# Kernel tuning notes

Measured on AMD Instinct MI355X. Metric: run time of the kernel, lower is better.

## Reference

```python
import jax, jax.numpy as jnp
import numpy as np

B, N, H = 2, 2048, 1024
NUM_HEADS = 16
HEAD_DIM = H // NUM_HEADS
SCALE = HEAD_DIM ** -0.5


def setup_inputs() -> dict:
    key = jax.random.key(0)
    k1, k2, k3, k4 = jax.random.split(key, 4)
    s = 0.02
    return {
        "x": jax.random.normal(k1, (B, N, H), dtype=jnp.float32),
        "x2": jax.random.normal(k2, (B, N, H), dtype=jnp.float32),
        "Wqkv": jax.random.normal(k3, (H, 3 * H), dtype=jnp.float32) * s,
        "Wout": jax.random.normal(k4, (H, H), dtype=jnp.float32) * s,
        "bout": jnp.zeros((H,), dtype=jnp.float32),
    }


def _split_qkv(t):
    # t: [B, N, 3H] -> [3, B, h, N, d]
    b, n, _ = t.shape
    t = t.reshape(b, n, 3, NUM_HEADS, HEAD_DIM)
    return jnp.transpose(t, (2, 0, 3, 1, 4))


def reference(x, x2, Wqkv, Wout, bout):
    # shared qkv projection applied to both streams (bias=False)
    qkv2 = _split_qkv(x2 @ Wqkv)  # k, v from x2
    k, v = qkv2[1], qkv2[2]       # [B, h, N2, d]
    qkv1 = _split_qkv(x @ Wqkv)   # q from x
    q = qkv1[0]                   # [B, h, N, d]

    att = jax.nn.softmax(jnp.einsum("bhxd,bhyd->bhxy", q, k) * SCALE, axis=-1)
    out = jnp.einsum("bhxy,bhyd->bhxd", att, v)        # [B, h, N, d]
    out = jnp.transpose(out, (0, 2, 1, 3)).reshape(x.shape[0], x.shape[1], -1)
    return out @ Wout + bout
```

## Files before the change

kernel.cpp:

```cpp
#include <hip/hip_runtime.h>

#define B_ 2
#define N_ 2048
#define H_ 1024
#define NH_ 16
#define D_ 64

typedef _Float16 f16;
typedef _Float16 f16x4 __attribute__((ext_vector_type(4)));
typedef _Float16 f16x8 __attribute__((ext_vector_type(8)));
typedef float f32x4 __attribute__((ext_vector_type(4)));

#define MFMA16(a, b, c) __builtin_amdgcn_mfma_f32_16x16x32_f16((a), (b), (c), 0, 0, 0)
#define MFMA16K(a, b, c) __builtin_amdgcn_mfma_f32_16x16x16f16((a), (b), (c), 0, 0, 0)

__device__ __forceinline__ void cp16(void* lds, const void* g) {
  __builtin_amdgcn_global_load_lds(
      (const __attribute__((address_space(1))) void*)g,
      (__attribute__((address_space(3))) void*)lds, 16, 0, 0);
}

__global__ __launch_bounds__(256) void convf16(
    const float* __restrict__ a, const float* __restrict__ b,
    f16* __restrict__ ao, f16* __restrict__ bo) {
  const size_t i = ((size_t)blockIdx.x * 256 + threadIdx.x) * 8;
  const float* __restrict__ src = (blockIdx.y == 0) ? a : b;
  f16* __restrict__ dst = (blockIdx.y == 0) ? ao : bo;
  float4 v0 = ((const float4*)(src + i))[0];
  float4 v1 = ((const float4*)(src + i))[1];
  f16x8 o;
  o[0] = (f16)v0.x; o[1] = (f16)v0.y; o[2] = (f16)v0.z; o[3] = (f16)v0.w;
  o[4] = (f16)v1.x; o[5] = (f16)v1.y; o[6] = (f16)v1.z; o[7] = (f16)v1.w;
  *(f16x8*)(dst + i) = o;
}

__global__ __launch_bounds__(256) void transw(
    const float* __restrict__ W, f16* __restrict__ Wt, int rows, int ncols) {
  const int cb = blockIdx.x * 64, kb = blockIdx.y * 64;
  const int t = threadIdx.x;
  __shared__ f16 T[64][72];
  {
    const int k = t >> 2, c0 = (t & 3) * 16;
    const float* wp = W + (size_t)(kb + k) * ncols + cb + c0;
    float4 w0 = ((const float4*)wp)[0];
    float4 w1 = ((const float4*)wp)[1];
    float4 w2 = ((const float4*)wp)[2];
    float4 w3 = ((const float4*)wp)[3];
    T[c0 + 0][k] = (f16)w0.x;  T[c0 + 1][k] = (f16)w0.y;
    T[c0 + 2][k] = (f16)w0.z;  T[c0 + 3][k] = (f16)w0.w;
    T[c0 + 4][k] = (f16)w1.x;  T[c0 + 5][k] = (f16)w1.y;
    T[c0 + 6][k] = (f16)w1.z;  T[c0 + 7][k] = (f16)w1.w;
    T[c0 + 8][k] = (f16)w2.x;  T[c0 + 9][k] = (f16)w2.y;
    T[c0 + 10][k] = (f16)w2.z; T[c0 + 11][k] = (f16)w2.w;
    T[c0 + 12][k] = (f16)w3.x; T[c0 + 13][k] = (f16)w3.y;
    T[c0 + 14][k] = (f16)w3.z; T[c0 + 15][k] = (f16)w3.w;
  }
  __syncthreads();
  {
    const int c = t >> 2, k0 = (t & 3) * 16;
    f16* op = Wt + (size_t)(cb + c) * rows + kb + k0;
    *(f16x8*)(op + 0) = *(const f16x8*)(&T[c][k0]);
    *(f16x8*)(op + 8) = *(const f16x8*)(&T[c][k0 + 8]);
  }
}

__global__ __launch_bounds__(256) void transv(
    const f16* __restrict__ V, f16* __restrict__ Vt) {
  const int nb = blockIdx.x * 64, bh = blockIdx.y;
  const int t = threadIdx.x;
  __shared__ f16 T[64][72];
  {
    const int n = t >> 2, d0 = (t & 3) * 16;
    const f16* vp = V + ((size_t)bh * N_ + nb + n) * D_ + d0;
    f16x8 v0 = *(const f16x8*)(vp);
    f16x8 v1 = *(const f16x8*)(vp + 8);
#pragma unroll
    for (int i = 0; i < 8; ++i) T[d0 + i][n] = v0[i];
#pragma unroll
    for (int i = 0; i < 8; ++i) T[d0 + 8 + i][n] = v1[i];
  }
  __syncthreads();
  {
    const int d = t >> 2, n0 = (t & 3) * 16;
    f16* op = Vt + ((size_t)bh * D_ + d) * N_ + nb + n0;
    *(f16x8*)(op + 0) = *(const f16x8*)(&T[d][n0]);
    *(f16x8*)(op + 8) = *(const f16x8*)(&T[d][n0 + 8]);
  }
}

__global__ __launch_bounds__(256) void qkv_mfma(
    const f16* __restrict__ Xc, const f16* __restrict__ X2c,
    const f16* __restrict__ Wt, f16* __restrict__ Qo,
    f16* __restrict__ Ko, f16* __restrict__ Vo) {
  const int bid = blockIdx.x;
  const int rb = (bid & 31) * 128;
  const int cb = (bid >> 5) * 128;
  const int t = threadIdx.x;
  const int lane = t & 63, wid = t >> 6;
  const int quad = lane >> 4, n16 = lane & 15;
  const int wm = wid >> 1, wn = wid & 1;

  const f16* __restrict__ A = (cb < H_) ? Xc : X2c;
  const int seg = cb >> 10;
  const float qscale = (seg == 0) ? 0.125f * 1.44269504f : 1.0f;
  f16* __restrict__ outp = (seg == 0) ? Qo : (seg == 1 ? Ko : Vo);

  __shared__ f16 As[128 * 32];
  __shared__ f16 Bs[128 * 32];

  f32x4 acc[4][4];
#pragma unroll
  for (int i = 0; i < 4; ++i)
#pragma unroll
    for (int j = 0; j < 4; ++j) acc[i][j] = (f32x4){0.f, 0.f, 0.f, 0.f};

  int srow0 = wid * 16 + (lane >> 2);
  int srow1 = 64 + srow0;
  int gl0 = ((lane & 3) ^ ((srow0 >> 1) & 3)) * 8;
  int gl1 = ((lane & 3) ^ ((srow1 >> 1) & 3)) * 8;
  const f16* gA0 = A + (size_t)(rb + srow0) * H_ + gl0;
  const f16* gA1 = A + (size_t)(rb + srow1) * H_ + gl1;
  const f16* gB0 = Wt + (size_t)(cb + srow0) * H_ + gl0;
  const f16* gB1 = Wt + (size_t)(cb + srow1) * H_ + gl1;
  f16* lA0 = &As[wid * 512];
  f16* lA1 = &As[2048 + wid * 512];
  f16* lB0 = &Bs[wid * 512];
  f16* lB1 = &Bs[2048 + wid * 512];

  const int fsw = (quad ^ ((n16 >> 1) & 3)) * 8;
  int aoff[4], boff[4];
#pragma unroll
  for (int i = 0; i < 4; ++i) {
    aoff[i] = (wm * 64 + i * 16 + n16) * 32 + fsw;
    boff[i] = (wn * 64 + i * 16 + n16) * 32 + fsw;
  }

  for (int kt = 0; kt < H_; kt += 32) {
    __syncthreads();
    cp16(lA0, gA0); cp16(lA1, gA1);
    cp16(lB0, gB0); cp16(lB1, gB1);
    gA0 += 32; gA1 += 32; gB0 += 32; gB1 += 32;
    __syncthreads();

    f16x8 af[4], bf[4];
#pragma unroll
    for (int mt = 0; mt < 4; ++mt) af[mt] = *(const f16x8*)(&As[aoff[mt]]);
#pragma unroll
    for (int nt = 0; nt < 4; ++nt) bf[nt] = *(const f16x8*)(&Bs[boff[nt]]);
#pragma unroll
    for (int mt = 0; mt < 4; ++mt)
#pragma unroll
      for (int nt = 0; nt < 4; ++nt)
        acc[mt][nt] = MFMA16(af[mt], bf[nt], acc[mt][nt]);
  }

#pragma unroll
  for (int mt = 0; mt < 4; ++mt)
#pragma unroll
    for (int nt = 0; nt < 4; ++nt)
#pragma unroll
      for (int r = 0; r < 4; ++r) {
        int grow = rb + wm * 64 + mt * 16 + quad * 4 + r;
        int gcol = cb + wn * 64 + nt * 16 + n16;
        int bb = grow >> 11, nn = grow & 2047;
        int hh = (gcol >> 6) & 15, dd = gcol & 63;
        outp[(((size_t)(bb * NH_ + hh)) * N_ + nn) * D_ + dd] =
            (f16)(acc[mt][nt][r] * qscale);
      }
}

__global__ __launch_bounds__(256) void attn4(
    const f16* __restrict__ Q, const f16* __restrict__ K,
    const f16* __restrict__ Vt, f16* __restrict__ AO) {
  const int bh = blockIdx.y;
  const int b = bh >> 4, h = bh & 15;
  const int qb = blockIdx.x * 64;
  const int t = threadIdx.x;
  const int lane = t & 63, wid = t >> 6;
  const int quad = lane >> 4, n16 = lane & 15;
  const int qh = wid & 1;
  const int kh = wid >> 1;

  const f16* __restrict__ Qp = Q + (size_t)bh * N_ * D_;
  const f16* __restrict__ Kp = K + (size_t)bh * N_ * D_;
  const f16* __restrict__ Vp = Vt + (size_t)bh * D_ * N_;

  __shared__ f16 Ks[2][64 * 64];
  __shared__ f16 Vs[2][64 * 64];

  f16x8 qf[2][2];
#pragma unroll
  for (int qc = 0; qc < 2; ++qc) {
    const f16* qp = Qp + (size_t)(qb + qh * 32 + qc * 16 + n16) * D_ + quad * 8;
    qf[qc][0] = *(const f16x8*)(qp);
    qf[qc][1] = *(const f16x8*)(qp + 32);
  }

  f32x4 o[2][4];
#pragma unroll
  for (int i = 0; i < 2; ++i)
#pragma unroll
    for (int j = 0; j < 4; ++j) o[i][j] = (f32x4){0.f, 0.f, 0.f, 0.f};
  float lsum[2] = {0.f, 0.f};

  const int srow0 = wid * 8 + (lane >> 3);
  const int srow1 = 32 + srow0;
  const int gl0 = ((lane & 7) ^ (srow0 & 7)) * 8;
  const int gl1 = ((lane & 7) ^ (srow1 & 7)) * 8;
  const f16* gK0 = Kp + (size_t)srow0 * D_ + gl0;
  const f16* gK1 = Kp + (size_t)srow1 * D_ + gl1;
  const f16* gV0 = Vp + (size_t)srow0 * N_ + gl0;
  const f16* gV1 = Vp + (size_t)srow1 * N_ + gl1;

  const int fs0 = (quad ^ (n16 & 7)) * 8;
  const int fs1 = ((quad + 4) ^ (n16 & 7)) * 8;
  int voff[4];
#pragma unroll
  for (int kc = 0; kc < 4; ++kc)
    voff[kc] = n16 * 64 + (((kc * 2 + (quad >> 1)) ^ (n16 & 7)) * 8) + (quad & 1) * 4;

  const f16* __restrict__ ks = &Ks[kh][0];
  const f16* __restrict__ vs = &Vs[kh][0];

  for (int kt = 0; kt < N_; kt += 128) {
    __syncthreads();
    cp16(&Ks[0][wid * 512], gK0 + (size_t)kt * D_);
    cp16(&Ks[0][2048 + wid * 512], gK1 + (size_t)kt * D_);
    cp16(&Ks[1][wid * 512], gK0 + (size_t)(kt + 64) * D_);
    cp16(&Ks[1][2048 + wid * 512], gK1 + (size_t)(kt + 64) * D_);
    cp16(&Vs[0][wid * 512], gV0 + kt);
    cp16(&Vs[0][2048 + wid * 512], gV1 + kt);
    cp16(&Vs[1][wid * 512], gV0 + kt + 64);
    cp16(&Vs[1][2048 + wid * 512], gV1 + kt + 64);
    __syncthreads();

    f32x4 s[2][4];
#pragma unroll
    for (int kc = 0; kc < 4; ++kc) {
      const f16x8 kf0 = *(const f16x8*)(&ks[(kc * 16 + n16) * 64 + fs0]);
      const f16x8 kf1 = *(const f16x8*)(&ks[(kc * 16 + n16) * 64 + fs1]);
#pragma unroll
      for (int qc = 0; qc < 2; ++qc) {
        f32x4 sv = (f32x4){0.f, 0.f, 0.f, 0.f};
        sv = MFMA16(kf0, qf[qc][0], sv);
        sv = MFMA16(kf1, qf[qc][1], sv);
        s[qc][kc] = sv;
      }
    }

    f16x4 pa[2][4];
#pragma unroll
    for (int qc = 0; qc < 2; ++qc)
#pragma unroll
      for (int kc = 0; kc < 4; ++kc)
#pragma unroll
        for (int r = 0; r < 4; ++r) {
          float p = __builtin_amdgcn_exp2f(s[qc][kc][r]);
          lsum[qc] += p;
          pa[qc][kc][r] = (f16)p;
        }

#pragma unroll
    for (int kc = 0; kc < 4; ++kc)
#pragma unroll
      for (int dt = 0; dt < 4; ++dt) {
        const f16x4 vb = *(const f16x4*)(&vs[dt * 1024 + voff[kc]]);
        o[0][dt] = MFMA16K(pa[0][kc], vb, o[0][dt]);
        o[1][dt] = MFMA16K(pa[1][kc], vb, o[1][dt]);
      }
  }

  __syncthreads();
  float* red = (float*)&Ks[0][0];
  if (kh == 1) {
    float* p = red + ((size_t)qh * 64 + lane) * 36;
#pragma unroll
    for (int qc = 0; qc < 2; ++qc)
#pragma unroll
      for (int dt = 0; dt < 4; ++dt)
        *(f32x4*)(p + (qc * 4 + dt) * 4) = o[qc][dt];
    p[32] = lsum[0];
    p[33] = lsum[1];
  }
  __syncthreads();
  if (kh == 0) {
    const float* p = red + ((size_t)qh * 64 + lane) * 36;
#pragma unroll
    for (int qc = 0; qc < 2; ++qc)
#pragma unroll
      for (int dt = 0; dt < 4; ++dt) {
        f32x4 v = *(const f32x4*)(p + (qc * 4 + dt) * 4);
#pragma unroll
        for (int r = 0; r < 4; ++r) o[qc][dt][r] += v[r];
      }
    lsum[0] += p[32];
    lsum[1] += p[33];

#pragma unroll
    for (int qc = 0; qc < 2; ++qc) {
      lsum[qc] += __shfl_xor(lsum[qc], 16);
      lsum[qc] += __shfl_xor(lsum[qc], 32);
    }

#pragma unroll
    for (int qc = 0; qc < 2; ++qc)
#pragma unroll
      for (int r = 0; r < 4; ++r) {
        float inv = 1.0f / __shfl(lsum[qc], quad * 4 + r);
        int nrow = qb + qh * 32 + qc * 16 + quad * 4 + r;
        f16* aop = AO + ((size_t)(b * N_ + nrow)) * H_ + h * 64;
#pragma unroll
        for (int dt = 0; dt < 4; ++dt)
          aop[dt * 16 + n16] = (f16)(o[qc][dt][r] * inv);
      }
  }
}

__global__ __launch_bounds__(256) void out_mfma(
    const f16* __restrict__ A, const f16* __restrict__ Wt,
    const float* __restrict__ bias, float* __restrict__ out) {
  const int bid = blockIdx.x;
  const int rb = (bid & 31) * 128;
  const int cb = (bid >> 5) * 128;
  const int t = threadIdx.x;
  const int lane = t & 63, wid = t >> 6;
  const int quad = lane >> 4, n16 = lane & 15;
  const int wm = wid >> 1, wn = wid & 1;

  __shared__ f16 As[128 * 32];
  __shared__ f16 Bs[128 * 32];

  f32x4 acc[4][4];
#pragma unroll
  for (int i = 0; i < 4; ++i)
#pragma unroll
    for (int j = 0; j < 4; ++j) acc[i][j] = (f32x4){0.f, 0.f, 0.f, 0.f};

  int srow0 = wid * 16 + (lane >> 2);
  int srow1 = 64 + srow0;
  int gl0 = ((lane & 3) ^ ((srow0 >> 1) & 3)) * 8;
  int gl1 = ((lane & 3) ^ ((srow1 >> 1) & 3)) * 8;
  const f16* gA0 = A + (size_t)(rb + srow0) * H_ + gl0;
  const f16* gA1 = A + (size_t)(rb + srow1) * H_ + gl1;
  const f16* gB0 = Wt + (size_t)(cb + srow0) * H_ + gl0;
  const f16* gB1 = Wt + (size_t)(cb + srow1) * H_ + gl1;
  f16* lA0 = &As[wid * 512];
  f16* lA1 = &As[2048 + wid * 512];
  f16* lB0 = &Bs[wid * 512];
  f16* lB1 = &Bs[2048 + wid * 512];

  const int fsw = (quad ^ ((n16 >> 1) & 3)) * 8;
  int aoff[4], boff[4];
#pragma unroll
  for (int i = 0; i < 4; ++i) {
    aoff[i] = (wm * 64 + i * 16 + n16) * 32 + fsw;
    boff[i] = (wn * 64 + i * 16 + n16) * 32 + fsw;
  }

  for (int kt = 0; kt < H_; kt += 32) {
    __syncthreads();
    cp16(lA0, gA0); cp16(lA1, gA1);
    cp16(lB0, gB0); cp16(lB1, gB1);
    gA0 += 32; gA1 += 32; gB0 += 32; gB1 += 32;
    __syncthreads();

    f16x8 af[4], bf[4];
#pragma unroll
    for (int mt = 0; mt < 4; ++mt) af[mt] = *(const f16x8*)(&As[aoff[mt]]);
#pragma unroll
    for (int nt = 0; nt < 4; ++nt) bf[nt] = *(const f16x8*)(&Bs[boff[nt]]);
#pragma unroll
    for (int mt = 0; mt < 4; ++mt)
#pragma unroll
      for (int nt = 0; nt < 4; ++nt)
        acc[mt][nt] = MFMA16(af[mt], bf[nt], acc[mt][nt]);
  }

#pragma unroll
  for (int nt = 0; nt < 4; ++nt) {
    int gcol = cb + wn * 64 + nt * 16 + n16;
    float bv = bias[gcol];
#pragma unroll
    for (int mt = 0; mt < 4; ++mt)
#pragma unroll
      for (int r = 0; r < 4; ++r) {
        int grow = rb + wm * 64 + mt * 16 + quad * 4 + r;
        out[(size_t)grow * H_ + gcol] = acc[mt][nt][r] + bv;
      }
  }
}

extern "C" void kernel_launch(void* const* d_in, const int* in_sizes, int n_in,
                              void* d_out, int out_size, void* d_ws, size_t ws_size,
                              hipStream_t stream) {
  const float* x    = (const float*)d_in[0];
  const float* x2   = (const float*)d_in[1];
  const float* Wqkv = (const float*)d_in[2];
  const float* Wout = (const float*)d_in[3];
  const float* bout = (const float*)d_in[4];
  float* out = (float*)d_out;

  const size_t per = (size_t)B_ * NH_ * N_ * D_;
  f16* Xc    = (f16*)d_ws;
  f16* X2c   = Xc + per;
  f16* Qw    = X2c + per;
  f16* Kw    = Qw + per;
  f16* Vw    = Kw + per;
  f16* Vtw   = Vw + per;
  f16* AO    = Vtw + per;
  f16* WqkvT = AO + per;
  f16* WoutT = WqkvT + (size_t)3072 * 1024;

  convf16<<<dim3(2048, 2), 256, 0, stream>>>(x, x2, Xc, X2c);
  transw<<<dim3(48, 16), 256, 0, stream>>>(Wqkv, WqkvT, H_, 3 * H_);
  transw<<<dim3(16, 16), 256, 0, stream>>>(Wout, WoutT, H_, H_);
  qkv_mfma<<<dim3(768), 256, 0, stream>>>(Xc, X2c, WqkvT, Qw, Kw, Vw);
  transv<<<dim3(32, 32), 256, 0, stream>>>(Vw, Vtw);
  attn4<<<dim3(32, 32), 256, 0, stream>>>(Qw, Kw, Vtw, AO);
  out_mfma<<<dim3(256), 256, 0, stream>>>(AO, WoutT, bout, out);
}
```

Baseline: 217.9 us.

## Merge prep kernels, emit transposed V from QKV GEMM, MFMA row sums in attention

```diff
diff --git a/kernel.cpp b/kernel.cpp
--- a/kernel.cpp
+++ b/kernel.cpp
@@ -7,6 +7,7 @@
 #define D_ 64
 
 typedef _Float16 f16;
+typedef _Float16 f16x2 __attribute__((ext_vector_type(2)));
 typedef _Float16 f16x4 __attribute__((ext_vector_type(4)));
 typedef _Float16 f16x8 __attribute__((ext_vector_type(8)));
 typedef float f32x4 __attribute__((ext_vector_type(4)));
@@ -20,24 +21,48 @@
       (__attribute__((address_space(3))) void*)lds, 16, 0, 0);
 }
 
-__global__ __launch_bounds__(256) void convf16(
-    const float* __restrict__ a, const float* __restrict__ b,
-    f16* __restrict__ ao, f16* __restrict__ bo) {
-  const size_t i = ((size_t)blockIdx.x * 256 + threadIdx.x) * 8;
-  const float* __restrict__ src = (blockIdx.y == 0) ? a : b;
-  f16* __restrict__ dst = (blockIdx.y == 0) ? ao : bo;
-  float4 v0 = ((const float4*)(src + i))[0];
-  float4 v1 = ((const float4*)(src + i))[1];
-  f16x8 o;
-  o[0] = (f16)v0.x; o[1] = (f16)v0.y; o[2] = (f16)v0.z; o[3] = (f16)v0.w;
-  o[4] = (f16)v1.x; o[5] = (f16)v1.y; o[6] = (f16)v1.z; o[7] = (f16)v1.w;
-  *(f16x8*)(dst + i) = o;
-}
-
-__global__ __launch_bounds__(256) void transw(
-    const float* __restrict__ W, f16* __restrict__ Wt, int rows, int ncols) {
-  const int cb = blockIdx.x * 64, kb = blockIdx.y * 64;
+__device__ __forceinline__ f16x4 pk4(float a, float b, float c, float d) {
+  auto lo = __builtin_amdgcn_cvt_pkrtz(a, b);
+  auto hi = __builtin_amdgcn_cvt_pkrtz(c, d);
+  f16x4 r;
+  r[0] = (f16)lo[0]; r[1] = (f16)lo[1]; r[2] = (f16)hi[0]; r[3] = (f16)hi[1];
+  return r;
+}
+
+__global__ __launch_bounds__(256) void prep(
+    const float* __restrict__ x, const float* __restrict__ x2,
+    f16* __restrict__ xo, f16* __restrict__ x2o,
+    const float* __restrict__ Wqkv, f16* __restrict__ WqkvT,
+    const float* __restrict__ Wout, f16* __restrict__ WoutT) {
+  const int bid = blockIdx.x;
   const int t = threadIdx.x;
+
+  if (bid < 4096) {
+    const float* __restrict__ src = (bid < 2048) ? x : x2;
+    f16* __restrict__ dst = (bid < 2048) ? xo : x2o;
+    const size_t i = ((size_t)(bid & 2047) * 256 + t) * 8;
+    float4 v0 = ((const float4*)(src + i))[0];
+    float4 v1 = ((const float4*)(src + i))[1];
+    f16x8 o;
+    o[0] = (f16)v0.x; o[1] = (f16)v0.y; o[2] = (f16)v0.z; o[3] = (f16)v0.w;
+    o[4] = (f16)v1.x; o[5] = (f16)v1.y; o[6] = (f16)v1.z; o[7] = (f16)v1.w;
+    *(f16x8*)(dst + i) = o;
+    return;
+  }
+
+  const float* __restrict__ W;
+  f16* __restrict__ Wt;
+  int cb, kb, rows, ncols;
+  if (bid < 4864) {
+    int j = bid - 4096;
+    W = Wqkv; Wt = WqkvT; rows = H_; ncols = 3 * H_;
+    cb = (j % 48) * 64; kb = (j / 48) * 64;
+  } else {
+    int j = bid - 4864;
+    W = Wout; Wt = WoutT; rows = H_; ncols = H_;
+    cb = (j & 15) * 64; kb = (j >> 4) * 64;
+  }
+
   __shared__ f16 T[64][72];
   {
     const int k = t >> 2, c0 = (t & 3) * 16;
@@ -64,34 +89,10 @@
   }
 }
 
-__global__ __launch_bounds__(256) void transv(
-    const f16* __restrict__ V, f16* __restrict__ Vt) {
-  const int nb = blockIdx.x * 64, bh = blockIdx.y;
-  const int t = threadIdx.x;
-  __shared__ f16 T[64][72];
-  {
-    const int n = t >> 2, d0 = (t & 3) * 16;
-    const f16* vp = V + ((size_t)bh * N_ + nb + n) * D_ + d0;
-    f16x8 v0 = *(const f16x8*)(vp);
-    f16x8 v1 = *(const f16x8*)(vp + 8);
-#pragma unroll
-    for (int i = 0; i < 8; ++i) T[d0 + i][n] = v0[i];
-#pragma unroll
-    for (int i = 0; i < 8; ++i) T[d0 + 8 + i][n] = v1[i];
-  }
-  __syncthreads();
-  {
-    const int d = t >> 2, n0 = (t & 3) * 16;
-    f16* op = Vt + ((size_t)bh * D_ + d) * N_ + nb + n0;
-    *(f16x8*)(op + 0) = *(const f16x8*)(&T[d][n0]);
-    *(f16x8*)(op + 8) = *(const f16x8*)(&T[d][n0 + 8]);
-  }
-}
-
 __global__ __launch_bounds__(256) void qkv_mfma(
     const f16* __restrict__ Xc, const f16* __restrict__ X2c,
     const f16* __restrict__ Wt, f16* __restrict__ Qo,
-    f16* __restrict__ Ko, f16* __restrict__ Vo) {
+    f16* __restrict__ Ko, f16* __restrict__ Vto) {
   const int bid = blockIdx.x;
   const int rb = (bid & 31) * 128;
   const int cb = (bid >> 5) * 128;
@@ -103,7 +104,6 @@
   const f16* __restrict__ A = (cb < H_) ? Xc : X2c;
   const int seg = cb >> 10;
   const float qscale = (seg == 0) ? 0.125f * 1.44269504f : 1.0f;
-  f16* __restrict__ outp = (seg == 0) ? Qo : (seg == 1 ? Ko : Vo);
 
   __shared__ f16 As[128 * 32];
   __shared__ f16 Bs[128 * 32];
@@ -135,6 +135,7 @@
     boff[i] = (wn * 64 + i * 16 + n16) * 32 + fsw;
   }
 
+  const bool vseg = (seg == 2);
   for (int kt = 0; kt < H_; kt += 32) {
     __syncthreads();
     cp16(lA0, gA0); cp16(lA1, gA1);
@@ -147,29 +148,54 @@
     for (int mt = 0; mt < 4; ++mt) af[mt] = *(const f16x8*)(&As[aoff[mt]]);
 #pragma unroll
     for (int nt = 0; nt < 4; ++nt) bf[nt] = *(const f16x8*)(&Bs[boff[nt]]);
+    if (!vseg) {
+#pragma unroll
+      for (int mt = 0; mt < 4; ++mt)
+#pragma unroll
+        for (int nt = 0; nt < 4; ++nt)
+          acc[mt][nt] = MFMA16(af[mt], bf[nt], acc[mt][nt]);
+    } else {
+#pragma unroll
+      for (int mt = 0; mt < 4; ++mt)
+#pragma unroll
+        for (int nt = 0; nt < 4; ++nt)
+          acc[mt][nt] = MFMA16(bf[nt], af[mt], acc[mt][nt]);
+    }
+  }
+
+  if (!vseg) {
+    f16* __restrict__ outp = (seg == 0) ? Qo : Ko;
 #pragma unroll
     for (int mt = 0; mt < 4; ++mt)
 #pragma unroll
       for (int nt = 0; nt < 4; ++nt)
-        acc[mt][nt] = MFMA16(af[mt], bf[nt], acc[mt][nt]);
-  }
-
-#pragma unroll
-  for (int mt = 0; mt < 4; ++mt)
-#pragma unroll
-    for (int nt = 0; nt < 4; ++nt)
-#pragma unroll
-      for (int r = 0; r < 4; ++r) {
-        int grow = rb + wm * 64 + mt * 16 + quad * 4 + r;
-        int gcol = cb + wn * 64 + nt * 16 + n16;
-        int bb = grow >> 11, nn = grow & 2047;
-        int hh = (gcol >> 6) & 15, dd = gcol & 63;
-        outp[(((size_t)(bb * NH_ + hh)) * N_ + nn) * D_ + dd] =
-            (f16)(acc[mt][nt][r] * qscale);
-      }
-}
-
-__global__ __launch_bounds__(256) void attn4(
+#pragma unroll
+        for (int r = 0; r < 4; ++r) {
+          int grow = rb + wm * 64 + mt * 16 + quad * 4 + r;
+          int gcol = cb + wn * 64 + nt * 16 + n16;
+          int bb = grow >> 11, nn = grow & 2047;
+          int hh = (gcol >> 6) & 15, dd = gcol & 63;
+          outp[(((size_t)(bb * NH_ + hh)) * N_ + nn) * D_ + dd] =
+              (f16)(acc[mt][nt][r] * qscale);
+        }
+  } else {
+#pragma unroll
+    for (int mt = 0; mt < 4; ++mt)
+#pragma unroll
+      for (int nt = 0; nt < 4; ++nt)
+#pragma unroll
+        for (int r = 0; r < 4; ++r) {
+          int gcol = cb + wn * 64 + nt * 16 + quad * 4 + r;
+          int grow = rb + wm * 64 + mt * 16 + n16;
+          int bb = grow >> 11, nn = grow & 2047;
+          int hh = (gcol >> 6) & 15, dd = gcol & 63;
+          Vto[(((size_t)(bb * NH_ + hh)) * D_ + dd) * N_ + nn] =
+              (f16)acc[mt][nt][r];
+        }
+  }
+}
+
+__global__ __launch_bounds__(256) void attn5(
     const f16* __restrict__ Q, const f16* __restrict__ K,
     const f16* __restrict__ Vt, f16* __restrict__ AO) {
   const int bh = blockIdx.y;
@@ -201,7 +227,10 @@
   for (int i = 0; i < 2; ++i)
 #pragma unroll
     for (int j = 0; j < 4; ++j) o[i][j] = (f32x4){0.f, 0.f, 0.f, 0.f};
-  float lsum[2] = {0.f, 0.f};
+  f32x4 lacc[2];
+  lacc[0] = (f32x4){0.f, 0.f, 0.f, 0.f};
+  lacc[1] = (f32x4){0.f, 0.f, 0.f, 0.f};
+  const f16x4 onesb = (f16x4){(f16)1.f, (f16)1.f, (f16)1.f, (f16)1.f};
 
   const int srow0 = wid * 8 + (lane >> 3);
   const int srow1 = 32 + srow0;
@@ -252,13 +281,18 @@
 #pragma unroll
     for (int qc = 0; qc < 2; ++qc)
 #pragma unroll
-      for (int kc = 0; kc < 4; ++kc)
-#pragma unroll
-        for (int r = 0; r < 4; ++r) {
-          float p = __builtin_amdgcn_exp2f(s[qc][kc][r]);
-          lsum[qc] += p;
-          pa[qc][kc][r] = (f16)p;
-        }
+      for (int kc = 0; kc < 4; ++kc) {
+        float p0 = __builtin_amdgcn_exp2f(s[qc][kc][0]);
+        float p1 = __builtin_amdgcn_exp2f(s[qc][kc][1]);
+        float p2 = __builtin_amdgcn_exp2f(s[qc][kc][2]);
+        float p3 = __builtin_amdgcn_exp2f(s[qc][kc][3]);
+        pa[qc][kc] = pk4(p0, p1, p2, p3);
+      }
+#pragma unroll
+    for (int kc = 0; kc < 4; ++kc) {
+      lacc[0] = MFMA16K(pa[0][kc], onesb, lacc[0]);
+      lacc[1] = MFMA16K(pa[1][kc], onesb, lacc[1]);
+    }
 
 #pragma unroll
     for (int kc = 0; kc < 4; ++kc)
@@ -273,40 +307,36 @@
   __syncthreads();
   float* red = (float*)&Ks[0][0];
   if (kh == 1) {
-    float* p = red + ((size_t)qh * 64 + lane) * 36;
-#pragma unroll
-    for (int qc = 0; qc < 2; ++qc)
+    float* p = red + ((size_t)(qh * 64 + lane)) * 40;
+#pragma unroll
+    for (int qc = 0; qc < 2; ++qc) {
 #pragma unroll
       for (int dt = 0; dt < 4; ++dt)
         *(f32x4*)(p + (qc * 4 + dt) * 4) = o[qc][dt];
-    p[32] = lsum[0];
-    p[33] = lsum[1];
+      *(f32x4*)(p + 32 + qc * 4) = lacc[qc];
+    }
   }
   __syncthreads();
   if (kh == 0) {
-    const float* p = red + ((size_t)qh * 64 + lane) * 36;
-#pragma unroll
-    for (int qc = 0; qc < 2; ++qc)
+    const float* p = red + ((size_t)(qh * 64 + lane)) * 40;
+#pragma unroll
+    for (int qc = 0; qc < 2; ++qc) {
 #pragma unroll
       for (int dt = 0; dt < 4; ++dt) {
         f32x4 v = *(const f32x4*)(p + (qc * 4 + dt) * 4);
 #pragma unroll
         for (int r = 0; r < 4; ++r) o[qc][dt][r] += v[r];
       }
-    lsum[0] += p[32];
-    lsum[1] += p[33];
-
-#pragma unroll
-    for (int qc = 0; qc < 2; ++qc) {
-      lsum[qc] += __shfl_xor(lsum[qc], 16);
-      lsum[qc] += __shfl_xor(lsum[qc], 32);
+      f32x4 lv = *(const f32x4*)(p + 32 + qc * 4);
+#pragma unroll
+      for (int r = 0; r < 4; ++r) lacc[qc][r] += lv[r];
     }
 
 #pragma unroll
     for (int qc = 0; qc < 2; ++qc)
 #pragma unroll
       for (int r = 0; r < 4; ++r) {
-        float inv = 1.0f / __shfl(lsum[qc], quad * 4 + r);
+        float inv = 1.0f / lacc[qc][r];
         int nrow = qb + qh * 32 + qc * 16 + quad * 4 + r;
         f16* aop = AO + ((size_t)(b * N_ + nrow)) * H_ + h * 64;
 #pragma unroll
@@ -405,17 +435,13 @@
   f16* X2c   = Xc + per;
   f16* Qw    = X2c + per;
   f16* Kw    = Qw + per;
-  f16* Vw    = Kw + per;
-  f16* Vtw   = Vw + per;
+  f16* Vtw   = Kw + per;
   f16* AO    = Vtw + per;
   f16* WqkvT = AO + per;
   f16* WoutT = WqkvT + (size_t)3072 * 1024;
 
-  convf16<<<dim3(2048, 2), 256, 0, stream>>>(x, x2, Xc, X2c);
-  transw<<<dim3(48, 16), 256, 0, stream>>>(Wqkv, WqkvT, H_, 3 * H_);
-  transw<<<dim3(16, 16), 256, 0, stream>>>(Wout, WoutT, H_, H_);
-  qkv_mfma<<<dim3(768), 256, 0, stream>>>(Xc, X2c, WqkvT, Qw, Kw, Vw);
-  transv<<<dim3(32, 32), 256, 0, stream>>>(Vw, Vtw);
-  attn4<<<dim3(32, 32), 256, 0, stream>>>(Qw, Kw, Vtw, AO);
+  prep<<<dim3(5120), 256, 0, stream>>>(x, x2, Xc, X2c, Wqkv, WqkvT, Wout, WoutT);
+  qkv_mfma<<<dim3(768), 256, 0, stream>>>(Xc, X2c, WqkvT, Qw, Kw, Vtw);
+  attn5<<<dim3(32, 32), 256, 0, stream>>>(Qw, Kw, Vtw, AO);
   out_mfma<<<dim3(256), 256, 0, stream>>>(AO, WoutT, bout, out);
 }
```

New measurement: 214.3 us. About the same (-1.7%).
